# Performance work log

Measured on AMD Instinct MI355X. Metric: run time of the kernel, lower is better.

The kernel has to match this reference:

```python
import jax, jax.numpy as jnp
import numpy as np

B, O, C, HID, H, W = 4, 8, 256, 128, 64, 64
STEPS = 2  # message passing steps


def _conv3x3(x, w, b):
    # x: [N,Cin,H,W], w: [Cout,Cin,3,3]
    y = jax.lax.conv_general_dilated(x, w, window_strides=(1, 1), padding='SAME',
                                     dimension_numbers=('NCHW', 'OIHW', 'NCHW'))
    return y + b[None, :, None, None]


def setup_inputs() -> dict:
    key = jax.random.key(0)
    ks = jax.random.split(key, 6)
    return {
        'batch_node_feats': jax.random.normal(ks[0], (B, C, H, W), jnp.float32),
        'batch_previous_masks': jax.random.uniform(ks[1], (B, O, H, W), jnp.float32),
        'batch_valid_indices': jnp.ones((B, O), jnp.bool_),
        'batch_previous_states': jnp.zeros((B, O), jnp.float32),  # unused (use_temporal_features=False)
        'enc_w': jax.random.normal(ks[2], (HID, C + 1, 3, 3), jnp.float32) * 0.02,
        'enc_b': jnp.zeros((HID,), jnp.float32),
        'gcn_w': jax.random.normal(ks[3], (HID, 2 * HID, 3, 3), jnp.float32) * 0.02,
        'gcn_b': jnp.zeros((HID,), jnp.float32),
        'ro_w': jax.random.normal(ks[4], (1, C + HID, 3, 3), jnp.float32) * 0.02,
        'ro_b': jnp.zeros((1,), jnp.float32),
    }


def reference(batch_node_feats, batch_previous_masks, batch_valid_indices,
              batch_previous_states, enc_w, enc_b, gcn_w, gcn_b, ro_w, ro_b):
    # All objects valid (batch_valid_indices all True) -> fully vectorized over B and O.
    feats = jnp.broadcast_to(batch_node_feats[:, None], (B, O, C, H, W))
    # Mask encoder: per-object state from frame feats + previous object mask.
    enc_in = jnp.concatenate([feats, batch_previous_masks[:, :, None]], axis=2)
    states = jax.nn.relu(_conv3x3(enc_in.reshape(B * O, C + 1, H, W), enc_w, enc_b))
    states = states.reshape(B, O, HID, H, W)
    # Fully-connected message passing: neighbors of i = all objects except i.
    for _ in range(STEPS):
        agg = states.sum(axis=1, keepdims=True) - states  # sum over others
        gcn_in = jnp.concatenate([states, agg], axis=2).reshape(B * O, 2 * HID, H, W)
        states = jax.nn.relu(_conv3x3(gcn_in, gcn_w, gcn_b)).reshape(B, O, HID, H, W)
    # Readout: per-object mask logits -> sigmoid.
    ro_in = jnp.concatenate([feats, states], axis=2).reshape(B * O, C + HID, H, W)
    out_masks = jax.nn.sigmoid(_conv3x3(ro_in, ro_w, ro_b)).reshape(B, O, H, W)
    return out_masks  # out_states is None when use_temporal_features=False
```

## Files before the change

kernel.cpp:

```cpp
#include <hip/hip_runtime.h>
#include <math.h>


typedef unsigned short ushort_t;
typedef _Float16 f16x8 __attribute__((ext_vector_type(8)));
typedef float f32x4 __attribute__((ext_vector_type(4)));

#define GLDS(gsrc, ldst)                                                      \
    __builtin_amdgcn_global_load_lds(                                         \
        (const __attribute__((address_space(1))) unsigned int*)(gsrc),        \
        (__attribute__((address_space(3))) unsigned int*)(ldst), 16, 0, 0)

__device__ __forceinline__ ushort_t f2h(float f) {
    _Float16 h = (_Float16)f;
    return *(ushort_t*)&h;
}
__device__ __forceinline__ float h2f(ushort_t u) {
    _Float16 h = *(_Float16*)&u;
    return (float)h;
}

__global__ __launch_bounds__(256) void prep_all(
    const float* __restrict__ feats, const float* __restrict__ enc_w,
    const float* __restrict__ gcn_w, const float* __restrict__ ro_w,
    ushort_t* __restrict__ featsT, ushort_t* __restrict__ WencF,
    ushort_t* __restrict__ WgcnS, ushort_t* __restrict__ WgcnD,
    ushort_t* __restrict__ WroQ, ushort_t* __restrict__ WroS)
{
    __shared__ float tile[64][65];
    int bid = blockIdx.x, t = threadIdx.x;
    if (bid < 1024) {
        int pt = bid & 63, ct = (bid >> 6) & 3, img = bid >> 8;
        int px_l = t & 63;
        const float* src = feats + ((size_t)img * 256 + ct * 64) * 4096 + pt * 64;
#pragma unroll
        for (int j = 0; j < 16; ++j) {
            int ci_l = (t >> 6) + j * 4;
            tile[px_l][ci_l] = src[(size_t)ci_l * 4096 + px_l];
        }
        __syncthreads();
        int px = t >> 2;
#pragma unroll
        for (int j = 0; j < 2; ++j) {
            int c8 = ((t & 3) + j * 4) * 8;
            uint4 v; ushort_t* pv = (ushort_t*)&v;
#pragma unroll
            for (int k = 0; k < 8; ++k) pv[k] = f2h(tile[px][c8 + k]);
            int cc = ct * 2 + (c8 >> 5);
            *(uint4*)(featsT + ((size_t)img * 8 + cc) * 131072 +
                      (size_t)(pt * 64 + px) * 32 + (c8 & 31)) = v;
        }
        return;
    }
    int i = (bid - 1024) * 256 + t;
    if (i < 294912) {
        int ci32 = i & 31, co = (i >> 5) & 127, tc = i >> 12;
        int tt = tc >> 3, cc = tc & 7, ci = cc * 32 + ci32;
        WencF[i] = f2h(enc_w[(co * 257 + ci) * 9 + tt]);
    } else if (i < 442368) {
        int j = i - 294912;
        int ci32 = j & 31, co = (j >> 5) & 127, tc = j >> 12;
        int tt = tc >> 2, cc = tc & 3, ci = cc * 32 + ci32;
        WgcnS[j] = f2h(gcn_w[(co * 256 + 128 + ci) * 9 + tt]);
    } else if (i < 589824) {
        int j = i - 442368;
        int ci32 = j & 31, co = (j >> 5) & 127, tc = j >> 12;
        int tt = tc >> 2, cc = tc & 3, ci = cc * 32 + ci32;
        WgcnD[j] = f2h(gcn_w[(co * 256 + ci) * 9 + tt] -
                       gcn_w[(co * 256 + 128 + ci) * 9 + tt]);
    } else if (i < 592128) {
        int j = i - 589824;
        int k = j & 7, r = j >> 3;
        int tt = r % 9, cq = r / 9, q = cq & 3, cc = cq >> 2;
        WroQ[j] = f2h(ro_w[(cc * 32 + q * 8 + k) * 9 + tt]);
    } else if (i < 593280) {
        int j = i - 592128;
        int k = j & 7, r = j >> 3;
        int tt = r % 9, cq = r / 9, q = cq & 3, cc = cq >> 2;
        WroS[j] = f2h(ro_w[(256 + cc * 32 + q * 8 + k) * 9 + tt]);
    }
}

template<int NCCBLK, bool FUSE, bool SUMIN>
__global__ __launch_bounds__(256, 3) void conv_k(
    const ushort_t* __restrict__ x, const ushort_t* __restrict__ W,
    ushort_t* __restrict__ out,
    const ushort_t* __restrict__ addp, const float* __restrict__ bias,
    int ncc_img)
{
    __shared__ ushort_t raw[25088];
    ushort_t* xs = raw;
    ushort_t* wlds = raw + 16896;
    ushort_t* eb16 = raw;

    const int rp = blockIdx.x, img = blockIdx.y, kz = blockIdx.z;
    const int row0 = rp * 2;
    const int cc0 = kz * NCCBLK;
    const int nchunk = 9 * NCCBLK;
    const int tid = threadIdx.x;
    const int w = tid >> 6, lane = tid & 63, lq = lane >> 4, lr = lane & 15;
    const int cg = w >> 1, pg = w & 1;

    const size_t objstride = (size_t)ncc_img * 131072;
    const ushort_t* xb = SUMIN ? x + (size_t)img * 8 * objstride
                               : x + (size_t)img * objstride;
    const int aoff0 = (cg * 64 + lr) * 32 + (lq ^ ((lr >> 1) & 3)) * 8;

    if (tid < 64) {
        int b = tid >> 5, r = (tid >> 3) & 3, c = (tid >> 2) & 1, s = tid & 3;
        *(uint4*)(xs + b * 8448 + r * 2112 + (c ? 65 : 0) * 32 + s * 8) =
            make_uint4(0, 0, 0, 0);
    }

    f32x4 acc[4][4];
#pragma unroll
    for (int a = 0; a < 4; ++a)
#pragma unroll
        for (int p = 0; p < 4; ++p) acc[a][p] = (f32x4){0.f, 0.f, 0.f, 0.f};

    const int gy = row0 - 1 + w;
    const bool row_ok = (unsigned)gy < 64u;
#define STAGE_ACT(cc_, buf_)                                                    \
    {                                                                           \
        ushort_t* dstrow = xs + (buf_) * 8448 + w * 2112;                       \
        if (row_ok) {                                                           \
            const ushort_t* src = xb + (size_t)(cc_) * 131072 + (size_t)gy * 2048; \
            if constexpr (SUMIN) {                                              \
                _Pragma("unroll")                                               \
                for (int u_ = 0; u_ < 4; ++u_) {                                \
                    f16x8 a_ = {0, 0, 0, 0, 0, 0, 0, 0};                        \
                    _Pragma("unroll")                                           \
                    for (int o_ = 0; o_ < 8; ++o_)                              \
                        a_ = a_ + *(const f16x8*)(src + (size_t)o_ * objstride + \
                                                  u_ * 512 + lane * 8);         \
                    int colp_ = 1 + u_ * 16 + (lane >> 2);                      \
                    int ssw_ = (lane & 3) ^ ((colp_ >> 1) & 3);                 \
                    *(f16x8*)(dstrow + colp_ * 32 + ssw_ * 8) = a_;             \
                }                                                               \
            } else {                                                            \
                _Pragma("unroll")                                               \
                for (int u_ = 0; u_ < 4; ++u_) {                                \
                    int colp_ = 1 + u_ * 16 + (lane >> 2);                      \
                    int ssw_ = (lane & 3) ^ ((colp_ >> 1) & 3);                 \
                    GLDS(src + (size_t)(colp_ - 1) * 32 + ssw_ * 8,             \
                         dstrow + 32 + u_ * 512);                               \
                }                                                               \
            }                                                                   \
        } else {                                                                \
            _Pragma("unroll")                                                   \
            for (int u_ = 0; u_ < 4; ++u_)                                      \
                *(uint4*)(dstrow + 32 + u_ * 512 + lane * 8) =                  \
                    make_uint4(0, 0, 0, 0);                                     \
        }                                                                       \
    }
#define STAGE_W(t_, cc_, buf_)                                                  \
    {                                                                           \
        const ushort_t* src = W + ((size_t)((t_) * ncc_img + (cc_)) * 4096);    \
        ushort_t* dst = wlds + (buf_) * 4096;                                   \
        _Pragma("unroll")                                                       \
        for (int j_ = 0; j_ < 2; ++j_) {                                        \
            int co_ = (w * 2 + j_) * 16 + (lane >> 2);                          \
            int ssw_ = (lane & 3) ^ ((co_ >> 1) & 3);                           \
            GLDS(src + co_ * 32 + ssw_ * 8, dst + (w * 2 + j_) * 512);          \
        }                                                                       \
    }

    STAGE_ACT(cc0, 0);
    STAGE_W(0, cc0, 0);

    int kc = 0;
#pragma unroll
    for (int ccl = 0; ccl < NCCBLK; ++ccl) {
        const int cc = cc0 + ccl;
        const int xbuf = ccl & 1;
#pragma unroll
        for (int t = 0; t < 9; ++t, ++kc) {
            __syncthreads();
            if (kc + 1 < nchunk) {
                if (t == 8) {
                    STAGE_W(0, cc + 1, (kc + 1) & 1);
                    STAGE_ACT(cc + 1, (ccl + 1) & 1);
                } else {
                    STAGE_W(t + 1, cc, (kc + 1) & 1);
                }
            }
            const int dy = t / 3, dx = t - 3 * dy;
            const ushort_t* wl = wlds + (kc & 1) * 4096 + aoff0;
            const int colb = dx + lr;
            const int swb = lq ^ ((colb >> 1) & 3);
            const ushort_t* xl = xs + xbuf * 8448 + (pg + dy) * 2112 +
                                 colb * 32 + swb * 8;
            f16x8 A0 = *(const f16x8*)(wl);
            f16x8 A1 = *(const f16x8*)(wl + 512);
            f16x8 A2 = *(const f16x8*)(wl + 1024);
            f16x8 A3 = *(const f16x8*)(wl + 1536);
#pragma unroll
            for (int p = 0; p < 4; ++p) {
                f16x8 Bf = *(const f16x8*)(xl + p * 512);
                acc[0][p] = __builtin_amdgcn_mfma_f32_16x16x32_f16(A0, Bf, acc[0][p], 0, 0, 0);
                acc[1][p] = __builtin_amdgcn_mfma_f32_16x16x32_f16(A1, Bf, acc[1][p], 0, 0, 0);
                acc[2][p] = __builtin_amdgcn_mfma_f32_16x16x32_f16(A2, Bf, acc[2][p], 0, 0, 0);
                acc[3][p] = __builtin_amdgcn_mfma_f32_16x16x32_f16(A3, Bf, acc[3][p], 0, 0, 0);
            }
        }
    }

    ushort_t* obase = out + (size_t)(kz * gridDim.y + img) * 524288;
    const int b4 = img >> 3;
#pragma unroll
    for (int r = 0; r < 2; ++r) {
        __syncthreads();
        if (pg == r) {
#pragma unroll
            for (int cf = 0; cf < 4; ++cf)
#pragma unroll
                for (int pf = 0; pf < 4; ++pf) {
                    int px = pf * 16 + lr;
                    int co_l = cg * 64 + cf * 16 + lq * 4;
                    ushort_t pk[4];
#pragma unroll
                    for (int j = 0; j < 4; ++j) pk[j] = f2h(acc[cf][pf][j]);
                    *(uint2*)(eb16 + px * 136 + co_l) = *(uint2*)pk;
                }
        }
        __syncthreads();
#pragma unroll
        for (int k2 = 0; k2 < 4; ++k2) {
            int i = tid + k2 * 256;
            int px = i >> 4, c16 = i & 15;
            int pxg = (row0 + r) * 64 + px;
            size_t coff = (size_t)(c16 >> 2) * 131072 + (size_t)pxg * 32 + (c16 & 3) * 8;
            uint4 v = *(uint4*)(eb16 + px * 136 + c16 * 8);
            if constexpr (FUSE) {
                const ushort_t* vp = (const ushort_t*)&v;
                float vv[8];
#pragma unroll
                for (int k = 0; k < 8; ++k) vv[k] = h2f(vp[k]) + bias[c16 * 8 + k];
#pragma unroll
                for (int p = 0; p < 4; ++p) {
                    uint4 av = *(const uint4*)(addp + (size_t)(p * 4 + b4) * 524288 + coff);
                    const ushort_t* ap = (const ushort_t*)&av;
#pragma unroll
                    for (int k = 0; k < 8; ++k) vv[k] += h2f(ap[k]);
                }
                uint4 sv; ushort_t* sp = (ushort_t*)&sv;
#pragma unroll
                for (int k = 0; k < 8; ++k) sp[k] = f2h(fmaxf(vv[k], 0.f));
                *(uint4*)(obase + coff) = sv;
            } else {
                *(uint4*)(obase + coff) = v;
            }
        }
    }
#undef STAGE_ACT
#undef STAGE_W
}

__global__ __launch_bounds__(256) void enc_obj_ro(
    const float* __restrict__ masks, const float* __restrict__ enc_w,
    const float* __restrict__ enc_b, const ushort_t* __restrict__ U1p,
    const ushort_t* __restrict__ featsT, const ushort_t* __restrict__ WroQ,
    ushort_t* __restrict__ S, ushort_t* __restrict__ USum,
    float* __restrict__ YR)
{
    int bid = blockIdx.x, tid = threadIdx.x;
    if (bid >= 1024) {
        int i = (bid - 1024) * 256 + tid;
        int cu = i & 31, px = (i >> 5) & 4095, b = i >> 17;
        int cc = cu >> 2, q = cu & 3;
        int y = px >> 6, xcol = px & 63;
        const ushort_t* wp = WroQ + (size_t)(cc * 4 + q) * 72;
        float wreg[9][8];
#pragma unroll
        for (int t = 0; t < 9; ++t) {
            uint4 wv = *(const uint4*)(wp + t * 8);
            const ushort_t* wq = (const ushort_t*)&wv;
#pragma unroll
            for (int k = 0; k < 8; ++k) wreg[t][k] = h2f(wq[k]);
        }
        const ushort_t* fb = featsT + (size_t)(b * 8 + cc) * 131072 + q * 8;
        float acc = 0.f;
#pragma unroll
        for (int dy = 0; dy < 3; ++dy) {
            int gy = y + dy - 1;
            if ((unsigned)gy >= 64u) continue;
#pragma unroll
            for (int dx = 0; dx < 3; ++dx) {
                int gx = xcol + dx - 1;
                if ((unsigned)gx >= 64u) continue;
                uint4 v = *(const uint4*)(fb + (size_t)(gy * 64 + gx) * 32);
                const ushort_t* vp = (const ushort_t*)&v;
#pragma unroll
                for (int k = 0; k < 8; ++k)
                    acc = fmaf(h2f(vp[k]), wreg[dy * 3 + dx][k], acc);
            }
        }
#pragma unroll
        for (int d = 16; d >= 1; d >>= 1) acc += __shfl_down(acc, d, 32);
        if (cu == 0) YR[b * 4096 + px] = acc;
        return;
    }
    int i = bid * 256 + tid;
    int s = i & 3, px = (i >> 2) & 4095, cc = (i >> 14) & 3, b = i >> 16;
    int co = cc * 32 + s * 8;
    int y = px >> 6, xx = px & 63;
    size_t coff = (size_t)cc * 131072 + (size_t)px * 32 + s * 8;
    float base[8];
#pragma unroll
    for (int k = 0; k < 8; ++k) base[k] = enc_b[co + k];
#pragma unroll
    for (int p = 0; p < 4; ++p) {
        uint4 v = *(const uint4*)(U1p + (size_t)(p * 4 + b) * 524288 + coff);
        const ushort_t* vp = (const ushort_t*)&v;
#pragma unroll
        for (int k = 0; k < 8; ++k) base[k] += h2f(vp[k]);
    }
    float wm[8][9];
#pragma unroll
    for (int k = 0; k < 8; ++k) {
        const float* wp = enc_w + (size_t)((co + k) * 257 + 256) * 9;
#pragma unroll
        for (int t = 0; t < 9; ++t) wm[k][t] = wp[t];
    }
    float sacc[8] = {0, 0, 0, 0, 0, 0, 0, 0};
#pragma unroll
    for (int o = 0; o < 8; ++o) {
        const float* m = masks + (size_t)(b * 8 + o) * 4096;
        float mt[9];
#pragma unroll
        for (int dy = 0; dy < 3; ++dy)
#pragma unroll
            for (int dx = 0; dx < 3; ++dx) {
                int gy_ = y + dy - 1, gx = xx + dx - 1;
                mt[dy * 3 + dx] =
                    ((unsigned)gy_ < 64u && (unsigned)gx < 64u) ? m[gy_ * 64 + gx] : 0.f;
            }
        uint4 sv; ushort_t* sp = (ushort_t*)&sv;
#pragma unroll
        for (int k = 0; k < 8; ++k) {
            float acc = base[k];
#pragma unroll
            for (int t = 0; t < 9; ++t) acc = fmaf(mt[t], wm[k][t], acc);
            acc = fmaxf(acc, 0.f);
            sacc[k] += acc;
            sp[k] = f2h(acc);
        }
        *(uint4*)(S + (size_t)(b * 8 + o) * 524288 + coff) = sv;
    }
    uint4 sv; ushort_t* sp = (ushort_t*)&sv;
#pragma unroll
    for (int k = 0; k < 8; ++k) sp[k] = f2h(sacc[k]);
    *(uint4*)(USum + (size_t)b * 524288 + coff) = sv;
}

__global__ __launch_bounds__(256) void ro_obj(
    const ushort_t* __restrict__ S, const ushort_t* __restrict__ WroS,
    const float* __restrict__ ro_b, const float* __restrict__ YR,
    float* __restrict__ out)
{
    int i = blockIdx.x * 256 + threadIdx.x;
    int cu = i & 15, px = (i >> 4) & 4095, n = i >> 16;
    int b = n >> 3;
    int cc = cu >> 2, q = cu & 3;
    int y = px >> 6, xcol = px & 63;
    const ushort_t* wp = WroS + (size_t)(cc * 4 + q) * 72;
    float wreg[9][8];
#pragma unroll
    for (int t = 0; t < 9; ++t) {
        uint4 wv = *(const uint4*)(wp + t * 8);
        const ushort_t* wq = (const ushort_t*)&wv;
#pragma unroll
        for (int k = 0; k < 8; ++k) wreg[t][k] = h2f(wq[k]);
    }
    const ushort_t* sb = S + ((size_t)n * 4 + cc) * 131072 + q * 8;
    float acc = 0.f;
#pragma unroll
    for (int dy = 0; dy < 3; ++dy) {
        int gy = y + dy - 1;
        if ((unsigned)gy >= 64u) continue;
#pragma unroll
        for (int dx = 0; dx < 3; ++dx) {
            int gx = xcol + dx - 1;
            if ((unsigned)gx >= 64u) continue;
            uint4 v = *(const uint4*)(sb + (size_t)(gy * 64 + gx) * 32);
            const ushort_t* vp = (const ushort_t*)&v;
#pragma unroll
            for (int k = 0; k < 8; ++k)
                acc = fmaf(h2f(vp[k]), wreg[dy * 3 + dx][k], acc);
        }
    }
#pragma unroll
    for (int d = 8; d >= 1; d >>= 1) acc += __shfl_down(acc, d, 16);
    if (cu == 0) {
        float v = acc + YR[b * 4096 + px] + ro_b[0];
        out[n * 4096 + px] = 1.f / (1.f + __expf(-v));
    }
}

extern "C" void kernel_launch(void* const* d_in, const int* in_sizes, int n_in,
                              void* d_out, int out_size, void* d_ws, size_t ws_size,
                              hipStream_t stream)
{
    const float* feats = (const float*)d_in[0];
    const float* masks = (const float*)d_in[1];
    const float* enc_w = (const float*)d_in[4];
    const float* enc_b = (const float*)d_in[5];
    const float* gcn_w = (const float*)d_in[6];
    const float* gcn_b = (const float*)d_in[7];
    const float* ro_w  = (const float*)d_in[8];
    const float* ro_b  = (const float*)d_in[9];
    float* out = (float*)d_out;

    ushort_t* WencF  = (ushort_t*)d_ws;
    ushort_t* WgcnS  = WencF + 294912;
    ushort_t* WgcnD  = WgcnS + 147456;
    ushort_t* WroQ   = WgcnD + 147456;
    ushort_t* WroS   = WroQ + 2304;
    ushort_t* featsT = WroS + 1152;
    ushort_t* Sa     = featsT + 4194304;
    ushort_t* Sb     = Sa + 16777216;
    ushort_t* USum   = Sb + 16777216;
    ushort_t* U1p16  = USum + 2097152;
    ushort_t* U2p16  = U1p16 + 8388608;
    float*    YR     = (float*)(U2p16 + 8388608);

    dim3 blk(256);

    prep_all<<<3344, blk, 0, stream>>>(feats, enc_w, gcn_w, ro_w,
                                       featsT, WencF, WgcnS, WgcnD, WroQ, WroS);

    conv_k<2, false, false><<<dim3(32, 4, 4), blk, 0, stream>>>(
        featsT, WencF, U1p16, nullptr, nullptr, 8);
    enc_obj_ro<<<3072, blk, 0, stream>>>(masks, enc_w, enc_b, U1p16,
                                         featsT, WroQ, Sa, USum, YR);

    conv_k<1, false, false><<<dim3(32, 4, 4), blk, 0, stream>>>(
        USum, WgcnS, U2p16, nullptr, nullptr, 4);
    conv_k<4, true, false><<<dim3(32, 32, 1), blk, 0, stream>>>(
        Sa, WgcnD, Sb, U2p16, gcn_b, 4);

    conv_k<1, false, true><<<dim3(32, 4, 4), blk, 0, stream>>>(
        Sb, WgcnS, U2p16, nullptr, nullptr, 4);
    conv_k<4, true, false><<<dim3(32, 32, 1), blk, 0, stream>>>(
        Sb, WgcnD, Sa, U2p16, gcn_b, 4);

    ro_obj<<<8192, blk, 0, stream>>>(Sa, WroS, ro_b, YR, out);
}
```

Baseline: 266.6 us.

## Add dedicated 4-row conv kernel for GCN diagonal convolutions with larger output tiles

Introduces a specialized conv_k4 kernel in which each block computes all 128 output channels over four image rows of one object. Its 4x8 MFMA accumulator tile per wave reuses each weight fragment across eight pixel fragments. Weight and activation tiles are double-buffered in LDS, and bias, the summed-neighbour term and ReLU are fused into the epilogue. The grid halves from 1024 to 512 blocks, and the large accumulator array raises register pressure, which may reduce occupancy despite the launch bound of two blocks per CU.

```diff
diff --git a/kernel.cpp b/kernel.cpp
--- a/kernel.cpp
+++ b/kernel.cpp
@@ -256,6 +256,149 @@
 #undef STAGE_W
 }
 
+__global__ __launch_bounds__(256, 2) void conv_k4(
+    const ushort_t* __restrict__ x, const ushort_t* __restrict__ W,
+    ushort_t* __restrict__ out, const ushort_t* __restrict__ addp,
+    const float* __restrict__ bias)
+{
+    __shared__ ushort_t raw[32768];
+    ushort_t* xs = raw;
+    ushort_t* wlds = raw + 24576;
+    ushort_t* eb16 = raw;
+
+    const int rq = blockIdx.x, img = blockIdx.y;
+    const int row0 = rq * 4;
+    const int tid = threadIdx.x;
+    const int w = tid >> 6, lane = tid & 63, lq = lane >> 4, lr = lane & 15;
+    const int cg = w >> 1, pg = w & 1;
+
+    const ushort_t* xb = x + (size_t)img * 524288;
+    const int aoff0 = (cg * 64 + lr) * 32 + (lq ^ ((lr >> 1) & 3)) * 8;
+
+    f32x4 acc[4][8];
+#pragma unroll
+    for (int a = 0; a < 4; ++a)
+#pragma unroll
+        for (int p = 0; p < 8; ++p) acc[a][p] = (f32x4){0.f, 0.f, 0.f, 0.f};
+
+#define STAGE_ACT4(cc_, buf_)                                                   \
+    {                                                                           \
+        const ushort_t* srcb = xb + (size_t)(cc_) * 131072;                     \
+        _Pragma("unroll")                                                       \
+        for (int j_ = 0; j_ < 6; ++j_) {                                        \
+            int idx_ = w * 6 + j_, rl_ = idx_ >> 2, q_ = idx_ & 3;              \
+            int gy_ = row0 - 1 + rl_;                                           \
+            ushort_t* dst_ = xs + (buf_) * 12288 + rl_ * 2048 + q_ * 512;       \
+            if ((unsigned)gy_ < 64u) {                                          \
+                int col_ = q_ * 16 + (lane >> 2);                               \
+                int ss_ = (lane & 3) ^ ((col_ >> 1) & 3);                       \
+                GLDS(srcb + (size_t)gy_ * 2048 + col_ * 32 + ss_ * 8, dst_);    \
+            } else {                                                            \
+                *(uint4*)(dst_ + lane * 8) = make_uint4(0, 0, 0, 0);            \
+            }                                                                   \
+        }                                                                       \
+    }
+#define STAGE_W4(t_, cc_, buf_)                                                 \
+    {                                                                           \
+        const ushort_t* src = W + ((size_t)((t_) * 4 + (cc_)) * 4096);          \
+        ushort_t* dst = wlds + (buf_) * 4096;                                   \
+        _Pragma("unroll")                                                       \
+        for (int j_ = 0; j_ < 2; ++j_) {                                        \
+            int co_ = (w * 2 + j_) * 16 + (lane >> 2);                          \
+            int ssw_ = (lane & 3) ^ ((co_ >> 1) & 3);                           \
+            GLDS(src + co_ * 32 + ssw_ * 8, dst + (w * 2 + j_) * 512);          \
+        }                                                                       \
+    }
+
+    STAGE_ACT4(0, 0);
+    STAGE_W4(0, 0, 0);
+
+#pragma unroll 1
+    for (int ccl = 0; ccl < 4; ++ccl) {
+        const int xbuf = ccl & 1;
+        const ushort_t* xbb = xs + xbuf * 12288;
+#pragma unroll
+        for (int t = 0; t < 9; ++t) {
+            const int kc = ccl * 9 + t;
+            __syncthreads();
+            if (t == 8) {
+                if (ccl < 3) {
+                    STAGE_W4(0, ccl + 1, (kc + 1) & 1);
+                    STAGE_ACT4(ccl + 1, (ccl + 1) & 1);
+                }
+            } else {
+                STAGE_W4(t + 1, ccl, (kc + 1) & 1);
+            }
+            const int dy = t / 3, dx = t - 3 * dy;
+            const ushort_t* wl = wlds + (kc & 1) * 4096 + aoff0;
+            f16x8 A0 = *(const f16x8*)(wl);
+            f16x8 A1 = *(const f16x8*)(wl + 512);
+            f16x8 A2 = *(const f16x8*)(wl + 1024);
+            f16x8 A3 = *(const f16x8*)(wl + 1536);
+#pragma unroll
+            for (int pf = 0; pf < 8; ++pf) {
+                const int rl = 2 * pg + (pf >> 2) + dy;
+                const int c = (pf & 3) * 16 + lr + dx - 1;
+                const int c2 = c < 0 ? 0 : (c > 63 ? 63 : c);
+                f16x8 Bf = *(const f16x8*)(xbb + rl * 2048 + c2 * 32 +
+                                           (lq ^ ((c2 >> 1) & 3)) * 8);
+                if (c != c2) Bf = (f16x8){0, 0, 0, 0, 0, 0, 0, 0};
+                acc[0][pf] = __builtin_amdgcn_mfma_f32_16x16x32_f16(A0, Bf, acc[0][pf], 0, 0, 0);
+                acc[1][pf] = __builtin_amdgcn_mfma_f32_16x16x32_f16(A1, Bf, acc[1][pf], 0, 0, 0);
+                acc[2][pf] = __builtin_amdgcn_mfma_f32_16x16x32_f16(A2, Bf, acc[2][pf], 0, 0, 0);
+                acc[3][pf] = __builtin_amdgcn_mfma_f32_16x16x32_f16(A3, Bf, acc[3][pf], 0, 0, 0);
+            }
+        }
+    }
+
+    ushort_t* obase = out + (size_t)img * 524288;
+    const int b4 = img >> 3;
+#pragma unroll
+    for (int r = 0; r < 4; ++r) {
+        __syncthreads();
+        if (pg == (r >> 1)) {
+            const int pb = (r & 1) * 4;
+#pragma unroll
+            for (int cf = 0; cf < 4; ++cf)
+#pragma unroll
+                for (int pf2 = 0; pf2 < 4; ++pf2) {
+                    int px = pf2 * 16 + lr;
+                    int co_l = cg * 64 + cf * 16 + lq * 4;
+                    ushort_t pk[4];
+#pragma unroll
+                    for (int j = 0; j < 4; ++j) pk[j] = f2h(acc[cf][pb + pf2][j]);
+                    *(uint2*)(eb16 + px * 136 + co_l) = *(uint2*)pk;
+                }
+        }
+        __syncthreads();
+#pragma unroll
+        for (int k2 = 0; k2 < 4; ++k2) {
+            int i = tid + k2 * 256;
+            int px = i >> 4, c16 = i & 15;
+            int pxg = (row0 + r) * 64 + px;
+            size_t coff = (size_t)(c16 >> 2) * 131072 + (size_t)pxg * 32 + (c16 & 3) * 8;
+            uint4 v = *(uint4*)(eb16 + px * 136 + c16 * 8);
+            const ushort_t* vp = (const ushort_t*)&v;
+            float vv[8];
+#pragma unroll
+            for (int k = 0; k < 8; ++k) vv[k] = h2f(vp[k]) + bias[c16 * 8 + k];
+#pragma unroll
+            for (int p = 0; p < 4; ++p) {
+                uint4 av = *(const uint4*)(addp + (size_t)(p * 4 + b4) * 524288 + coff);
+                const ushort_t* ap = (const ushort_t*)&av;
+#pragma unroll
+                for (int k = 0; k < 8; ++k) vv[k] += h2f(ap[k]);
+            }
+            uint4 sv; ushort_t* sp = (ushort_t*)&sv;
+#pragma unroll
+            for (int k = 0; k < 8; ++k) sp[k] = f2h(fmaxf(vv[k], 0.f));
+            *(uint4*)(obase + coff) = sv;
+        }
+    }
+#undef STAGE_ACT4
+#undef STAGE_W4
+}
+
 __global__ __launch_bounds__(256) void enc_obj_ro(
     const float* __restrict__ masks, const float* __restrict__ enc_w,
     const float* __restrict__ enc_b, const ushort_t* __restrict__ U1p,
@@ -436,13 +579,11 @@
 
     conv_k<1, false, false><<<dim3(32, 4, 4), blk, 0, stream>>>(
         USum, WgcnS, U2p16, nullptr, nullptr, 4);
-    conv_k<4, true, false><<<dim3(32, 32, 1), blk, 0, stream>>>(
-        Sa, WgcnD, Sb, U2p16, gcn_b, 4);
+    conv_k4<<<dim3(16, 32), blk, 0, stream>>>(Sa, WgcnD, Sb, U2p16, gcn_b);
 
     conv_k<1, false, true><<<dim3(32, 4, 4), blk, 0, stream>>>(
         Sb, WgcnS, U2p16, nullptr, nullptr, 4);
-    conv_k<4, true, false><<<dim3(32, 32, 1), blk, 0, stream>>>(
-        Sb, WgcnD, Sa, U2p16, gcn_b, 4);
+    conv_k4<<<dim3(16, 32), blk, 0, stream>>>(Sb, WgcnD, Sa, U2p16, gcn_b);
 
     ro_obj<<<8192, blk, 0, stream>>>(Sa, WroS, ro_b, YR, out);
 }
```

After: 295.0 us. 1.11x slower.

## Software-pipeline LDS fragment reads one tap ahead of MFMA in conv kernel

Applied to the files above, without the earlier changes.

Restructures the conv inner loop so the A (weight) and B (activation) fragments for the next tap are read from LDS into double-buffered registers before the current tap's MFMAs issue. Weight staging now runs two chunks ahead, and the next activation block is staged mid-block at tap 4 instead of at the block boundary. The goal is to hide LDS read latency behind matrix ops and to spread out global-to-LDS traffic. In exchange it uses more VGPRs for the prefetched fragments, and the buffer-index logic is more intricate, which risks races or lower occupancy.

```diff
diff --git a/kernel.cpp b/kernel.cpp
--- a/kernel.cpp
+++ b/kernel.cpp
@@ -164,43 +164,79 @@
             GLDS(src + co_ * 32 + ssw_ * 8, dst + (w * 2 + j_) * 512);          \
         }                                                                       \
     }
+#define AREAD(dst_, buf_)                                                       \
+    {                                                                           \
+        const ushort_t* wl_ = wlds + (buf_) * 4096 + aoff0;                     \
+        dst_[0] = *(const f16x8*)(wl_);                                         \
+        dst_[1] = *(const f16x8*)(wl_ + 512);                                   \
+        dst_[2] = *(const f16x8*)(wl_ + 1024);                                  \
+        dst_[3] = *(const f16x8*)(wl_ + 1536);                                  \
+    }
+#define BREAD(dst_, t_, xb_)                                                    \
+    {                                                                           \
+        const int dy_ = (t_) / 3, dx_ = (t_) - 3 * ((t_) / 3);                  \
+        const int colb_ = dx_ + lr;                                             \
+        const int swb_ = lq ^ ((colb_ >> 1) & 3);                               \
+        const ushort_t* xl_ = xs + (xb_) * 8448 + (pg + dy_) * 2112 +           \
+                              colb_ * 32 + swb_ * 8;                            \
+        dst_[0] = *(const f16x8*)(xl_);                                         \
+        dst_[1] = *(const f16x8*)(xl_ + 512);                                   \
+        dst_[2] = *(const f16x8*)(xl_ + 1024);                                  \
+        dst_[3] = *(const f16x8*)(xl_ + 1536);                                  \
+    }
+#define TAPMFMA(Asel_, Bsel_)                                                   \
+    {                                                                           \
+        _Pragma("unroll")                                                       \
+        for (int p = 0; p < 4; ++p) {                                           \
+            acc[0][p] = __builtin_amdgcn_mfma_f32_16x16x32_f16(Asel_[0], Bsel_[p], acc[0][p], 0, 0, 0); \
+            acc[1][p] = __builtin_amdgcn_mfma_f32_16x16x32_f16(Asel_[1], Bsel_[p], acc[1][p], 0, 0, 0); \
+            acc[2][p] = __builtin_amdgcn_mfma_f32_16x16x32_f16(Asel_[2], Bsel_[p], acc[2][p], 0, 0, 0); \
+            acc[3][p] = __builtin_amdgcn_mfma_f32_16x16x32_f16(Asel_[3], Bsel_[p], acc[3][p], 0, 0, 0); \
+        }                                                                       \
+    }
+
+    f16x8 Ap0[4], Ap1[4], Bp0[4], Bp1[4];
 
     STAGE_ACT(cc0, 0);
     STAGE_W(0, cc0, 0);
 
-    int kc = 0;
 #pragma unroll
     for (int ccl = 0; ccl < NCCBLK; ++ccl) {
         const int cc = cc0 + ccl;
         const int xbuf = ccl & 1;
 #pragma unroll
-        for (int t = 0; t < 9; ++t, ++kc) {
+        for (int t = 0; t < 9; ++t) {
+            const int kc = ccl * 9 + t;
             __syncthreads();
-            if (kc + 1 < nchunk) {
-                if (t == 8) {
-                    STAGE_W(0, cc + 1, (kc + 1) & 1);
-                    STAGE_ACT(cc + 1, (ccl + 1) & 1);
-                } else {
-                    STAGE_W(t + 1, cc, (kc + 1) & 1);
+            if (kc == 0) {
+                AREAD(Ap0, 0);
+                BREAD(Bp0, 0, 0);
+                if (nchunk > 1) BREAD(Bp1, 1, 0);
+                __syncthreads();
+                if (nchunk > 1) STAGE_W(1, cc0, 1);
+                if (nchunk > 2) STAGE_W(2, cc0, 0);
+                TAPMFMA(Ap0, Bp0);
+            } else if (kc == 1) {
+                AREAD(Ap1, 1);
+                if (2 < nchunk) { AREAD(Ap0, 0); BREAD(Bp0, 2, xbuf); }
+                __syncthreads();
+                if (3 < nchunk) STAGE_W(3, cc0, 1);
+                TAPMFMA(Ap1, Bp1);
+            } else {
+                if (kc + 2 < nchunk) {
+                    const int st = (kc + 2) % 9;
+                    const int scc = cc0 + (kc + 2) / 9;
+                    STAGE_W(st, scc, kc & 1);
                 }
-            }
-            const int dy = t / 3, dx = t - 3 * dy;
-            const ushort_t* wl = wlds + (kc & 1) * 4096 + aoff0;
-            const int colb = dx + lr;
-            const int swb = lq ^ ((colb >> 1) & 3);
-            const ushort_t* xl = xs + xbuf * 8448 + (pg + dy) * 2112 +
-                                 colb * 32 + swb * 8;
-            f16x8 A0 = *(const f16x8*)(wl);
-            f16x8 A1 = *(const f16x8*)(wl + 512);
-            f16x8 A2 = *(const f16x8*)(wl + 1024);
-            f16x8 A3 = *(const f16x8*)(wl + 1536);
-#pragma unroll
-            for (int p = 0; p < 4; ++p) {
-                f16x8 Bf = *(const f16x8*)(xl + p * 512);
-                acc[0][p] = __builtin_amdgcn_mfma_f32_16x16x32_f16(A0, Bf, acc[0][p], 0, 0, 0);
-                acc[1][p] = __builtin_amdgcn_mfma_f32_16x16x32_f16(A1, Bf, acc[1][p], 0, 0, 0);
-                acc[2][p] = __builtin_amdgcn_mfma_f32_16x16x32_f16(A2, Bf, acc[2][p], 0, 0, 0);
-                acc[3][p] = __builtin_amdgcn_mfma_f32_16x16x32_f16(A3, Bf, acc[3][p], 0, 0, 0);
+                if (t == 4 && ccl + 1 < NCCBLK) STAGE_ACT(cc + 1, xbuf ^ 1);
+                if (kc + 1 < nchunk) {
+                    const int nt = (t == 8) ? 0 : t + 1;
+                    const int nxb = (t == 8) ? (xbuf ^ 1) : xbuf;
+                    if (((kc + 1) & 1) == 0) { AREAD(Ap0, 0); BREAD(Bp0, nt, nxb); }
+                    else                     { AREAD(Ap1, 1); BREAD(Bp1, nt, nxb); }
+                }
+                if ((kc & 1) == 0) TAPMFMA(Ap0, Bp0)
+                else               TAPMFMA(Ap1, Bp1)
             }
         }
     }
@@ -254,6 +290,9 @@
     }
 #undef STAGE_ACT
 #undef STAGE_W
+#undef AREAD
+#undef BREAD
+#undef TAPMFMA
 }
 
 __global__ __launch_bounds__(256) void enc_obj_ro(
```

New measurement: 270.8 us. No clear change (+1.6%).

## Deepen conv mainloop prefetch to two stages with explicit vmcnt waits

Applied to the files above, without the earlier changes.

Restructures the implicit-GEMM conv mainloop so weight chunks are prefetched two steps ahead, and the next activation tile is staged mid-channel-block. Plain __syncthreads are replaced by fine-grained s_waitcnt vmcnt/lgkmcnt plus raw s_barrier, so the loop waits only for the loads it needs. All B fragments are loaded before the MFMA burst, which is wrapped in s_setprio. The aim is to hide global-to-LDS latency behind MFMA work, at the cost of fragile hand-counted wait values that could race if the load counts are wrong.

```diff
diff --git a/kernel.cpp b/kernel.cpp
--- a/kernel.cpp
+++ b/kernel.cpp
@@ -10,6 +10,11 @@
     __builtin_amdgcn_global_load_lds(                                         \
         (const __attribute__((address_space(1))) unsigned int*)(gsrc),        \
         (__attribute__((address_space(3))) unsigned int*)(ldst), 16, 0, 0)
+
+#define WAITVM0() asm volatile("s_waitcnt vmcnt(0)" ::: "memory")
+#define WAITVM2() asm volatile("s_waitcnt vmcnt(2)" ::: "memory")
+#define WAITVM6() asm volatile("s_waitcnt vmcnt(6)" ::: "memory")
+#define WAITLGKM0() asm volatile("s_waitcnt lgkmcnt(0)" ::: "memory")
 
 __device__ __forceinline__ ushort_t f2h(float f) {
     _Float16 h = (_Float16)f;
@@ -167,23 +172,21 @@
 
     STAGE_ACT(cc0, 0);
     STAGE_W(0, cc0, 0);
-
-    int kc = 0;
+    STAGE_W(1, cc0, 1);
+    WAITLGKM0();
+
 #pragma unroll
     for (int ccl = 0; ccl < NCCBLK; ++ccl) {
         const int cc = cc0 + ccl;
         const int xbuf = ccl & 1;
 #pragma unroll
-        for (int t = 0; t < 9; ++t, ++kc) {
-            __syncthreads();
-            if (kc + 1 < nchunk) {
-                if (t == 8) {
-                    STAGE_W(0, cc + 1, (kc + 1) & 1);
-                    STAGE_ACT(cc + 1, (ccl + 1) & 1);
-                } else {
-                    STAGE_W(t + 1, cc, (kc + 1) & 1);
-                }
-            }
+        for (int t = 0; t < 9; ++t) {
+            const int kc = ccl * 9 + t;
+            if (kc == nchunk - 1) { WAITVM0(); }
+            else if ((t == 5 || t == 6) && (ccl + 1 < NCCBLK)) { WAITVM6(); }
+            else { WAITVM2(); }
+            __builtin_amdgcn_s_barrier();
+
             const int dy = t / 3, dx = t - 3 * dy;
             const ushort_t* wl = wlds + (kc & 1) * 4096 + aoff0;
             const int colb = dx + lr;
@@ -194,14 +197,37 @@
             f16x8 A1 = *(const f16x8*)(wl + 512);
             f16x8 A2 = *(const f16x8*)(wl + 1024);
             f16x8 A3 = *(const f16x8*)(wl + 1536);
-#pragma unroll
-            for (int p = 0; p < 4; ++p) {
-                f16x8 Bf = *(const f16x8*)(xl + p * 512);
-                acc[0][p] = __builtin_amdgcn_mfma_f32_16x16x32_f16(A0, Bf, acc[0][p], 0, 0, 0);
-                acc[1][p] = __builtin_amdgcn_mfma_f32_16x16x32_f16(A1, Bf, acc[1][p], 0, 0, 0);
-                acc[2][p] = __builtin_amdgcn_mfma_f32_16x16x32_f16(A2, Bf, acc[2][p], 0, 0, 0);
-                acc[3][p] = __builtin_amdgcn_mfma_f32_16x16x32_f16(A3, Bf, acc[3][p], 0, 0, 0);
+            f16x8 B0 = *(const f16x8*)(xl);
+            f16x8 B1 = *(const f16x8*)(xl + 512);
+            f16x8 B2 = *(const f16x8*)(xl + 1024);
+            f16x8 B3 = *(const f16x8*)(xl + 1536);
+
+            if (kc + 2 < nchunk) {
+                WAITLGKM0();
+                __builtin_amdgcn_sched_barrier(0);
+                __builtin_amdgcn_s_barrier();
+                STAGE_W((kc + 2) % 9, cc0 + (kc + 2) / 9, kc & 1);
+                if (t == 4 && ccl + 1 < NCCBLK) STAGE_ACT(cc + 1, xbuf ^ 1);
             }
+
+            __builtin_amdgcn_s_setprio(1);
+            acc[0][0] = __builtin_amdgcn_mfma_f32_16x16x32_f16(A0, B0, acc[0][0], 0, 0, 0);
+            acc[1][0] = __builtin_amdgcn_mfma_f32_16x16x32_f16(A1, B0, acc[1][0], 0, 0, 0);
+            acc[2][0] = __builtin_amdgcn_mfma_f32_16x16x32_f16(A2, B0, acc[2][0], 0, 0, 0);
+            acc[3][0] = __builtin_amdgcn_mfma_f32_16x16x32_f16(A3, B0, acc[3][0], 0, 0, 0);
+            acc[0][1] = __builtin_amdgcn_mfma_f32_16x16x32_f16(A0, B1, acc[0][1], 0, 0, 0);
+            acc[1][1] = __builtin_amdgcn_mfma_f32_16x16x32_f16(A1, B1, acc[1][1], 0, 0, 0);
+            acc[2][1] = __builtin_amdgcn_mfma_f32_16x16x32_f16(A2, B1, acc[2][1], 0, 0, 0);
+            acc[3][1] = __builtin_amdgcn_mfma_f32_16x16x32_f16(A3, B1, acc[3][1], 0, 0, 0);
+            acc[0][2] = __builtin_amdgcn_mfma_f32_16x16x32_f16(A0, B2, acc[0][2], 0, 0, 0);
+            acc[1][2] = __builtin_amdgcn_mfma_f32_16x16x32_f16(A1, B2, acc[1][2], 0, 0, 0);
+            acc[2][2] = __builtin_amdgcn_mfma_f32_16x16x32_f16(A2, B2, acc[2][2], 0, 0, 0);
+            acc[3][2] = __builtin_amdgcn_mfma_f32_16x16x32_f16(A3, B2, acc[3][2], 0, 0, 0);
+            acc[0][3] = __builtin_amdgcn_mfma_f32_16x16x32_f16(A0, B3, acc[0][3], 0, 0, 0);
+            acc[1][3] = __builtin_amdgcn_mfma_f32_16x16x32_f16(A1, B3, acc[1][3], 0, 0, 0);
+            acc[2][3] = __builtin_amdgcn_mfma_f32_16x16x32_f16(A2, B3, acc[2][3], 0, 0, 0);
+            acc[3][3] = __builtin_amdgcn_mfma_f32_16x16x32_f16(A3, B3, acc[3][3], 0, 0, 0);
+            __builtin_amdgcn_s_setprio(0);
         }
     }
 
```

After: 267.5 us. No clear change (+0.3%).
